# Kernel optimization log

Hardware: AMD Instinct MI355X
Metric: run time of the kernel (lower is better)

## Reference

```python
import jax, jax.numpy as jnp
import numpy as np


def setup_inputs() -> dict:
    key = jax.random.key(0)
    k1, k2, k3, k4, k5 = jax.random.split(key, 5)
    B, Tx, Ty, E, D = 8, 256, 256, 256, 256
    return {
        "encoder_out_seq": jax.random.normal(k1, (B, Tx, E), dtype=jnp.float32),
        "decoder_out_seq": jax.random.normal(k2, (B, Ty, D), dtype=jnp.float32),
        "W_a": jax.random.normal(k3, (E, E), dtype=jnp.float32) * 0.05,
        "U_a": jax.random.normal(k4, (D, E), dtype=jnp.float32) * 0.05,
        "V_a": jax.random.normal(k5, (E, 1), dtype=jnp.float32) * 0.05,
    }


def reference(encoder_out_seq, decoder_out_seq, W_a, U_a, V_a):
    # encoder_out_seq: [B, Tx, E], decoder_out_seq: [B, Ty, D]
    # Vectorized Bahdanau additive attention (the K.rnn scan is a fake
    # recurrence: each timestep only uses the per-step decoder input and the
    # constant encoder sequence).
    W_dot_s = jnp.einsum("bxe,ef->bxf", encoder_out_seq, W_a)   # [B, Tx, E]
    U_dot_h = jnp.einsum("byd,de->bye", decoder_out_seq, U_a)   # [B, Ty, E]
    # [B, Ty, Tx, E] broadcast add + tanh, then project with V_a -> [B, Ty, Tx]
    Ws_plus_Uh = jnp.tanh(W_dot_s[:, None, :, :] + U_dot_h[:, :, None, :])
    e = jnp.einsum("byxe,eo->byx", Ws_plus_Uh, V_a)             # [B, Ty, Tx]
    e = jax.nn.softmax(e, axis=-1)                               # softmax over Tx
    # context: weighted sum of encoder states -> [B, Ty, E]
    c = jnp.einsum("byx,bxe->bye", e, encoder_out_seq)
    return (c, e)
```

## Files before the change

### kernel.cpp

```cpp
#include <hip/hip_runtime.h>
#include <cstddef>
#include <stdint.h>

#define NB 8
#define TX 256
#define TY 256
#define NE 256

#define CSC 2.8853900817779268f

__device__ __forceinline__ void gload_lds16(const float* g, float* l) {
    __builtin_amdgcn_global_load_lds(
        (const __attribute__((address_space(1))) void*)g,
        (__attribute__((address_space(3))) void*)l,
        16, 0, 0);
}

__global__ __launch_bounds__(512) void prep_kernel(
    const float* __restrict__ enc, const float* __restrict__ dec,
    const float* __restrict__ Wa, const float* __restrict__ Ua,
    float* __restrict__ ZwT, float* __restrict__ Zu)
{
    const int tx = threadIdx.x;
    const int w  = threadIdx.y;
    const int tid = w * 64 + tx;
    int blk = blockIdx.x;
    const bool isU = blk >= 128;
    if (isU) blk -= 128;
    const int b  = blk >> 4;
    const int r0 = (blk & 15) * 16;

    __shared__ float rowsL[16 * NE];
    __shared__ float MbL[2][16 * NE];
    __shared__ float tL[16][260];

    const float* M = isU ? Ua : Wa;

    gload_lds16(M + tid * 4,        MbL[0] + w * 256);
    gload_lds16(M + 2048 + tid * 4, MbL[0] + 2048 + w * 256);
    const float* src = (isU ? dec : enc) + ((size_t)b * 256 + r0) * NE;
    ((float4*)rowsL)[tid]       = ((const float4*)src)[tid];
    ((float4*)rowsL)[tid + 512] = ((const float4*)src)[tid + 512];
    __syncthreads();

    const int e0 = tx * 4;
    const int rA = w * 2, rB = w * 2 + 1;
    float4 acc0 = make_float4(0.f, 0.f, 0.f, 0.f);
    float4 acc1 = make_float4(0.f, 0.f, 0.f, 0.f);
    const float* rowA = rowsL + rA * NE;
    const float* rowB = rowsL + rB * NE;

    for (int c = 0; c < 16; ++c) {
        if (c < 15) {
            const float* g = M + (size_t)(c + 1) * 4096;
            float* dst = MbL[(c + 1) & 1];
            gload_lds16(g + tid * 4,        dst + w * 256);
            gload_lds16(g + 2048 + tid * 4, dst + 2048 + w * 256);
        }
        const float* mb = MbL[c & 1] + e0;
        const int kbase = c * 16;
        #pragma unroll
        for (int j = 0; j < 16; ++j) {
            const float4 mw = *(const float4*)(mb + j * NE);
            const float a = rowA[kbase + j];
            const float d = rowB[kbase + j];
            acc0.x = __builtin_fmaf(a, mw.x, acc0.x);
            acc0.y = __builtin_fmaf(a, mw.y, acc0.y);
            acc0.z = __builtin_fmaf(a, mw.z, acc0.z);
            acc0.w = __builtin_fmaf(a, mw.w, acc0.w);
            acc1.x = __builtin_fmaf(d, mw.x, acc1.x);
            acc1.y = __builtin_fmaf(d, mw.y, acc1.y);
            acc1.z = __builtin_fmaf(d, mw.z, acc1.z);
            acc1.w = __builtin_fmaf(d, mw.w, acc1.w);
        }
        __syncthreads();
    }

    acc0.x = __builtin_amdgcn_exp2f(acc0.x * CSC);
    acc0.y = __builtin_amdgcn_exp2f(acc0.y * CSC);
    acc0.z = __builtin_amdgcn_exp2f(acc0.z * CSC);
    acc0.w = __builtin_amdgcn_exp2f(acc0.w * CSC);
    acc1.x = __builtin_amdgcn_exp2f(acc1.x * CSC);
    acc1.y = __builtin_amdgcn_exp2f(acc1.y * CSC);
    acc1.z = __builtin_amdgcn_exp2f(acc1.z * CSC);
    acc1.w = __builtin_amdgcn_exp2f(acc1.w * CSC);

    if (isU) {
        *(float4*)(Zu + ((size_t)b * TY + r0 + rA) * NE + e0) = acc0;
        *(float4*)(Zu + ((size_t)b * TY + r0 + rB) * NE + e0) = acc1;
    } else {
        *(float4*)&tL[rA][e0] = acc0;
        *(float4*)&tL[rB][e0] = acc1;
        __syncthreads();
        #pragma unroll
        for (int rep = 0; rep < 2; ++rep) {
            const int f4id = tid + rep * 512;
            const int e  = f4id >> 2;
            const int xq = (f4id & 3) * 4;
            float4 o;
            o.x = tL[xq + 0][e];
            o.y = tL[xq + 1][e];
            o.z = tL[xq + 2][e];
            o.w = tL[xq + 3][e];
            *(float4*)(ZwT + (size_t)b * NE * TX + (size_t)e * TX + r0 + xq) = o;
        }
    }
}

__global__ __launch_bounds__(512, 4) void attn_kernel(
    const float* __restrict__ enc, const float* __restrict__ ZwT,
    const float* __restrict__ Zu, const float* __restrict__ Va,
    float* __restrict__ c_out, float* __restrict__ e_out)
{
    const int tx = threadIdx.x;
    const int w  = threadIdx.y;
    const int tid = w * 64 + tx;
    const int b  = blockIdx.x & 7;
    const int y0 = (blockIdx.x >> 3) * 4;

    __shared__ float4 zu4L[NE];
    __shared__ float  vL[NE];
    __shared__ float4 accL[8][4][64];
    __shared__ float  pL4[TX][4];

    {
        const int e = tid & 255;
        if (tid < 256) {
            const float* zp = Zu + ((size_t)b * TY + y0) * NE + e;
            zu4L[e] = make_float4(zp[0], zp[NE], zp[2 * NE], zp[3 * NE]);
        } else {
            vL[e] = Va[e];
        }
    }
    __syncthreads();

    const float* wp = ZwT + (size_t)b * NE * TX + (size_t)(w * 32) * TX + tx * 4;
    const float4* zup = &zu4L[w * 32];
    const float*  vp  = &vL[w * 32];
    float4 acc0 = make_float4(0.f, 0.f, 0.f, 0.f);
    float4 acc1 = acc0, acc2 = acc0, acc3 = acc0;
    #pragma unroll 4
    for (int e = 0; e < 32; ++e) {
        const float4 zw  = *(const float4*)(wp + (size_t)e * TX);
        const float4 zu4 = zup[e];
        const float  v   = vp[e];
        acc0.x = __builtin_fmaf(v, __builtin_amdgcn_rcpf(__builtin_fmaf(zw.x, zu4.x, 1.f)), acc0.x);
        acc0.y = __builtin_fmaf(v, __builtin_amdgcn_rcpf(__builtin_fmaf(zw.y, zu4.x, 1.f)), acc0.y);
        acc0.z = __builtin_fmaf(v, __builtin_amdgcn_rcpf(__builtin_fmaf(zw.z, zu4.x, 1.f)), acc0.z);
        acc0.w = __builtin_fmaf(v, __builtin_amdgcn_rcpf(__builtin_fmaf(zw.w, zu4.x, 1.f)), acc0.w);
        acc1.x = __builtin_fmaf(v, __builtin_amdgcn_rcpf(__builtin_fmaf(zw.x, zu4.y, 1.f)), acc1.x);
        acc1.y = __builtin_fmaf(v, __builtin_amdgcn_rcpf(__builtin_fmaf(zw.y, zu4.y, 1.f)), acc1.y);
        acc1.z = __builtin_fmaf(v, __builtin_amdgcn_rcpf(__builtin_fmaf(zw.z, zu4.y, 1.f)), acc1.z);
        acc1.w = __builtin_fmaf(v, __builtin_amdgcn_rcpf(__builtin_fmaf(zw.w, zu4.y, 1.f)), acc1.w);
        acc2.x = __builtin_fmaf(v, __builtin_amdgcn_rcpf(__builtin_fmaf(zw.x, zu4.z, 1.f)), acc2.x);
        acc2.y = __builtin_fmaf(v, __builtin_amdgcn_rcpf(__builtin_fmaf(zw.y, zu4.z, 1.f)), acc2.y);
        acc2.z = __builtin_fmaf(v, __builtin_amdgcn_rcpf(__builtin_fmaf(zw.z, zu4.z, 1.f)), acc2.z);
        acc2.w = __builtin_fmaf(v, __builtin_amdgcn_rcpf(__builtin_fmaf(zw.w, zu4.z, 1.f)), acc2.w);
        acc3.x = __builtin_fmaf(v, __builtin_amdgcn_rcpf(__builtin_fmaf(zw.x, zu4.w, 1.f)), acc3.x);
        acc3.y = __builtin_fmaf(v, __builtin_amdgcn_rcpf(__builtin_fmaf(zw.y, zu4.w, 1.f)), acc3.y);
        acc3.z = __builtin_fmaf(v, __builtin_amdgcn_rcpf(__builtin_fmaf(zw.z, zu4.w, 1.f)), acc3.z);
        acc3.w = __builtin_fmaf(v, __builtin_amdgcn_rcpf(__builtin_fmaf(zw.w, zu4.w, 1.f)), acc3.w);
    }
    accL[w][0][tx] = acc0;
    accL[w][1][tx] = acc1;
    accL[w][2][tx] = acc2;
    accL[w][3][tx] = acc3;
    __syncthreads();

    const int yy = w & 3;
    float4 s = make_float4(0.f, 0.f, 0.f, 0.f);
    #pragma unroll
    for (int ww = 0; ww < 8; ++ww) {
        const float4 a = accL[ww][yy][tx];
        s.x += a.x; s.y += a.y; s.z += a.z; s.w += a.w;
    }
    s.x *= -2.f; s.y *= -2.f; s.z *= -2.f; s.w *= -2.f;

    float m = fmaxf(fmaxf(s.x, s.y), fmaxf(s.z, s.w));
    #pragma unroll
    for (int off = 32; off; off >>= 1) m = fmaxf(m, __shfl_xor(m, off));
    float4 p;
    p.x = __expf(s.x - m);
    p.y = __expf(s.y - m);
    p.z = __expf(s.z - m);
    p.w = __expf(s.w - m);
    float sum = (p.x + p.y) + (p.z + p.w);
    #pragma unroll
    for (int off = 32; off; off >>= 1) sum += __shfl_xor(sum, off);
    const float inv = __builtin_amdgcn_rcpf(sum);
    p.x *= inv; p.y *= inv; p.z *= inv; p.w *= inv;

    if (w < 4) {
        *(float4*)(e_out + ((size_t)b * TY + y0 + yy) * TX + tx * 4) = p;
        pL4[tx * 4 + 0][yy] = p.x;
        pL4[tx * 4 + 1][yy] = p.y;
        pL4[tx * 4 + 2][yy] = p.z;
        pL4[tx * 4 + 3][yy] = p.w;
    }
    __syncthreads();

    const float* ep = enc + (size_t)b * TX * NE + (size_t)(w * 32) * NE + tx * 4;
    float4 c0 = make_float4(0.f, 0.f, 0.f, 0.f);
    float4 c1 = c0, c2 = c0, c3 = c0;
    #pragma unroll 4
    for (int x = 0; x < 32; ++x) {
        const float4 ev = *(const float4*)(ep + (size_t)x * NE);
        const float4 p4 = *(const float4*)&pL4[w * 32 + x][0];
        c0.x = __builtin_fmaf(p4.x, ev.x, c0.x);
        c0.y = __builtin_fmaf(p4.x, ev.y, c0.y);
        c0.z = __builtin_fmaf(p4.x, ev.z, c0.z);
        c0.w = __builtin_fmaf(p4.x, ev.w, c0.w);
        c1.x = __builtin_fmaf(p4.y, ev.x, c1.x);
        c1.y = __builtin_fmaf(p4.y, ev.y, c1.y);
        c1.z = __builtin_fmaf(p4.y, ev.z, c1.z);
        c1.w = __builtin_fmaf(p4.y, ev.w, c1.w);
        c2.x = __builtin_fmaf(p4.z, ev.x, c2.x);
        c2.y = __builtin_fmaf(p4.z, ev.y, c2.y);
        c2.z = __builtin_fmaf(p4.z, ev.z, c2.z);
        c2.w = __builtin_fmaf(p4.z, ev.w, c2.w);
        c3.x = __builtin_fmaf(p4.w, ev.x, c3.x);
        c3.y = __builtin_fmaf(p4.w, ev.y, c3.y);
        c3.z = __builtin_fmaf(p4.w, ev.z, c3.z);
        c3.w = __builtin_fmaf(p4.w, ev.w, c3.w);
    }
    __syncthreads();
    accL[w][0][tx] = c0;
    accL[w][1][tx] = c1;
    accL[w][2][tx] = c2;
    accL[w][3][tx] = c3;
    __syncthreads();

    if (w < 4) {
        float4 cs = make_float4(0.f, 0.f, 0.f, 0.f);
        #pragma unroll
        for (int ww = 0; ww < 8; ++ww) {
            const float4 t = accL[ww][w][tx];
            cs.x += t.x; cs.y += t.y; cs.z += t.z; cs.w += t.w;
        }
        *(float4*)(c_out + ((size_t)b * TY + y0 + w) * NE + tx * 4) = cs;
    }
}

extern "C" void kernel_launch(void* const* d_in, const int* in_sizes, int n_in,
                              void* d_out, int out_size, void* d_ws, size_t ws_size,
                              hipStream_t stream) {
    const float* enc = (const float*)d_in[0];
    const float* dec = (const float*)d_in[1];
    const float* Wa  = (const float*)d_in[2];
    const float* Ua  = (const float*)d_in[3];
    const float* Va  = (const float*)d_in[4];

    float* c_out = (float*)d_out;
    float* e_out = (float*)d_out + (size_t)NB * TY * NE;

    float* ZwT = (float*)d_ws;
    float* Zu  = (float*)d_ws + (size_t)NB * NE * TX;

    prep_kernel<<<256, dim3(64, 8), 0, stream>>>(enc, dec, Wa, Ua, ZwT, Zu);
    attn_kernel<<<512, dim3(64, 8), 0, stream>>>(enc, ZwT, Zu, Va, c_out, e_out);
}
```

Before: 39.61 us.

## Process eight decoder rows per attention block and retile prep GEMM

The attention kernel now handles 8 decoder rows per block instead of 4, halving the grid to 256 blocks. Each ZwT and encoder load is reused across twice as many rows, and all 8 waves take part in the softmax, the stores and the context reduction. The prep kernel holds the input rows transposed in LDS, so each thread computes a 4-row by 2-column tile from float4 row reads. The trade-off is more registers per thread (occupancy hint lowered from 4 to 2), a larger LDS footprint and fewer blocks to spread across CUs.

```diff
diff --git a/kernel.cpp b/kernel.cpp
--- a/kernel.cpp
+++ b/kernel.cpp
@@ -30,25 +30,33 @@
     const int b  = blk >> 4;
     const int r0 = (blk & 15) * 16;
 
-    __shared__ float rowsL[16 * NE];
-    __shared__ float MbL[2][16 * NE];
+    const int rq = (w & 3) * 4;
+    const int eh = (w >> 2) * 128;
+    const int cc = eh + tx * 2;
+
+    __shared__ float rowsT[256][16];
+    __shared__ float MbL[2][16 * 256];
     __shared__ float tL[16][260];
 
     const float* M = isU ? Ua : Wa;
 
+    const float* src = (isU ? dec : enc) + ((size_t)b * 256 + r0) * NE;
+    #pragma unroll
+    for (int j = 0; j < 2; ++j) {
+        const int f   = tid + j * 512;
+        const int row = f & 15;
+        const int kq  = f >> 4;
+        const float4 v = ((const float4*)src)[row * 64 + kq];
+        rowsT[kq * 4 + 0][row] = v.x;
+        rowsT[kq * 4 + 1][row] = v.y;
+        rowsT[kq * 4 + 2][row] = v.z;
+        rowsT[kq * 4 + 3][row] = v.w;
+    }
     gload_lds16(M + tid * 4,        MbL[0] + w * 256);
     gload_lds16(M + 2048 + tid * 4, MbL[0] + 2048 + w * 256);
-    const float* src = (isU ? dec : enc) + ((size_t)b * 256 + r0) * NE;
-    ((float4*)rowsL)[tid]       = ((const float4*)src)[tid];
-    ((float4*)rowsL)[tid + 512] = ((const float4*)src)[tid + 512];
-    __syncthreads();
-
-    const int e0 = tx * 4;
-    const int rA = w * 2, rB = w * 2 + 1;
-    float4 acc0 = make_float4(0.f, 0.f, 0.f, 0.f);
-    float4 acc1 = make_float4(0.f, 0.f, 0.f, 0.f);
-    const float* rowA = rowsL + rA * NE;
-    const float* rowB = rowsL + rB * NE;
+    __syncthreads();
+
+    float2 a0 = make_float2(0.f, 0.f), a1 = a0, a2 = a0, a3 = a0;
 
     for (int c = 0; c < 16; ++c) {
         if (c < 15) {
@@ -57,57 +65,61 @@
             gload_lds16(g + tid * 4,        dst + w * 256);
             gload_lds16(g + 2048 + tid * 4, dst + 2048 + w * 256);
         }
-        const float* mb = MbL[c & 1] + e0;
+        const float* mb = MbL[c & 1] + cc;
         const int kbase = c * 16;
-        #pragma unroll
+        #pragma unroll 8
         for (int j = 0; j < 16; ++j) {
-            const float4 mw = *(const float4*)(mb + j * NE);
-            const float a = rowA[kbase + j];
-            const float d = rowB[kbase + j];
-            acc0.x = __builtin_fmaf(a, mw.x, acc0.x);
-            acc0.y = __builtin_fmaf(a, mw.y, acc0.y);
-            acc0.z = __builtin_fmaf(a, mw.z, acc0.z);
-            acc0.w = __builtin_fmaf(a, mw.w, acc0.w);
-            acc1.x = __builtin_fmaf(d, mw.x, acc1.x);
-            acc1.y = __builtin_fmaf(d, mw.y, acc1.y);
-            acc1.z = __builtin_fmaf(d, mw.z, acc1.z);
-            acc1.w = __builtin_fmaf(d, mw.w, acc1.w);
+            const float2 mw = *(const float2*)(mb + j * 256);
+            const float4 rv = *(const float4*)&rowsT[kbase + j][rq];
+            a0.x = __builtin_fmaf(rv.x, mw.x, a0.x);
+            a0.y = __builtin_fmaf(rv.x, mw.y, a0.y);
+            a1.x = __builtin_fmaf(rv.y, mw.x, a1.x);
+            a1.y = __builtin_fmaf(rv.y, mw.y, a1.y);
+            a2.x = __builtin_fmaf(rv.z, mw.x, a2.x);
+            a2.y = __builtin_fmaf(rv.z, mw.y, a2.y);
+            a3.x = __builtin_fmaf(rv.w, mw.x, a3.x);
+            a3.y = __builtin_fmaf(rv.w, mw.y, a3.y);
         }
         __syncthreads();
     }
 
-    acc0.x = __builtin_amdgcn_exp2f(acc0.x * CSC);
-    acc0.y = __builtin_amdgcn_exp2f(acc0.y * CSC);
-    acc0.z = __builtin_amdgcn_exp2f(acc0.z * CSC);
-    acc0.w = __builtin_amdgcn_exp2f(acc0.w * CSC);
-    acc1.x = __builtin_amdgcn_exp2f(acc1.x * CSC);
-    acc1.y = __builtin_amdgcn_exp2f(acc1.y * CSC);
-    acc1.z = __builtin_amdgcn_exp2f(acc1.z * CSC);
-    acc1.w = __builtin_amdgcn_exp2f(acc1.w * CSC);
+    a0.x = __builtin_amdgcn_exp2f(a0.x * CSC);
+    a0.y = __builtin_amdgcn_exp2f(a0.y * CSC);
+    a1.x = __builtin_amdgcn_exp2f(a1.x * CSC);
+    a1.y = __builtin_amdgcn_exp2f(a1.y * CSC);
+    a2.x = __builtin_amdgcn_exp2f(a2.x * CSC);
+    a2.y = __builtin_amdgcn_exp2f(a2.y * CSC);
+    a3.x = __builtin_amdgcn_exp2f(a3.x * CSC);
+    a3.y = __builtin_amdgcn_exp2f(a3.y * CSC);
 
     if (isU) {
-        *(float4*)(Zu + ((size_t)b * TY + r0 + rA) * NE + e0) = acc0;
-        *(float4*)(Zu + ((size_t)b * TY + r0 + rB) * NE + e0) = acc1;
+        const int rbase = r0 + rq;
+        *(float2*)(Zu + ((size_t)b * TY + rbase + 0) * NE + cc) = a0;
+        *(float2*)(Zu + ((size_t)b * TY + rbase + 1) * NE + cc) = a1;
+        *(float2*)(Zu + ((size_t)b * TY + rbase + 2) * NE + cc) = a2;
+        *(float2*)(Zu + ((size_t)b * TY + rbase + 3) * NE + cc) = a3;
     } else {
-        *(float4*)&tL[rA][e0] = acc0;
-        *(float4*)&tL[rB][e0] = acc1;
+        tL[rq + 0][cc] = a0.x; tL[rq + 0][cc + 1] = a0.y;
+        tL[rq + 1][cc] = a1.x; tL[rq + 1][cc + 1] = a1.y;
+        tL[rq + 2][cc] = a2.x; tL[rq + 2][cc + 1] = a2.y;
+        tL[rq + 3][cc] = a3.x; tL[rq + 3][cc + 1] = a3.y;
         __syncthreads();
         #pragma unroll
         for (int rep = 0; rep < 2; ++rep) {
-            const int f4id = tid + rep * 512;
-            const int e  = f4id >> 2;
-            const int xq = (f4id & 3) * 4;
+            const int f   = tid + rep * 512;
+            const int e   = f >> 2;
+            const int xq4 = (f & 3) * 4;
             float4 o;
-            o.x = tL[xq + 0][e];
-            o.y = tL[xq + 1][e];
-            o.z = tL[xq + 2][e];
-            o.w = tL[xq + 3][e];
-            *(float4*)(ZwT + (size_t)b * NE * TX + (size_t)e * TX + r0 + xq) = o;
-        }
-    }
-}
-
-__global__ __launch_bounds__(512, 4) void attn_kernel(
+            o.x = tL[xq4 + 0][e];
+            o.y = tL[xq4 + 1][e];
+            o.z = tL[xq4 + 2][e];
+            o.w = tL[xq4 + 3][e];
+            *(float4*)(ZwT + ((size_t)b * NE + e) * TX + r0 + xq4) = o;
+        }
+    }
+}
+
+__global__ __launch_bounds__(512, 2) void attn_kernel(
     const float* __restrict__ enc, const float* __restrict__ ZwT,
     const float* __restrict__ Zu, const float* __restrict__ Va,
     float* __restrict__ c_out, float* __restrict__ e_out)
@@ -116,62 +128,57 @@
     const int w  = threadIdx.y;
     const int tid = w * 64 + tx;
     const int b  = blockIdx.x & 7;
-    const int y0 = (blockIdx.x >> 3) * 4;
-
-    __shared__ float4 zu4L[NE];
+    const int y0 = (blockIdx.x >> 3) * 8;
+    const int y  = y0 + w;
+
+    __shared__ float4 zuLo[NE];
+    __shared__ float4 zuHi[NE];
     __shared__ float  vL[NE];
-    __shared__ float4 accL[8][4][64];
-    __shared__ float  pL4[TX][4];
+    __shared__ float4 accL[8][8][64];
+    __shared__ float  pLT[8][TX];
 
     {
         const int e = tid & 255;
+        const float* zp = Zu + ((size_t)b * TY + y0) * NE + e;
         if (tid < 256) {
-            const float* zp = Zu + ((size_t)b * TY + y0) * NE + e;
-            zu4L[e] = make_float4(zp[0], zp[NE], zp[2 * NE], zp[3 * NE]);
+            zuLo[e] = make_float4(zp[0], zp[NE], zp[2 * NE], zp[3 * NE]);
+            vL[e] = Va[e];
         } else {
-            vL[e] = Va[e];
+            zuHi[e] = make_float4(zp[4 * NE], zp[5 * NE], zp[6 * NE], zp[7 * NE]);
         }
     }
     __syncthreads();
 
     const float* wp = ZwT + (size_t)b * NE * TX + (size_t)(w * 32) * TX + tx * 4;
-    const float4* zup = &zu4L[w * 32];
-    const float*  vp  = &vL[w * 32];
-    float4 acc0 = make_float4(0.f, 0.f, 0.f, 0.f);
-    float4 acc1 = acc0, acc2 = acc0, acc3 = acc0;
+    float4 a0 = make_float4(0.f, 0.f, 0.f, 0.f);
+    float4 a1 = a0, a2 = a0, a3 = a0, a4 = a0, a5 = a0, a6 = a0, a7 = a0;
+
+#define SC(A, ZU) \
+    A.x = __builtin_fmaf(v, __builtin_amdgcn_rcpf(__builtin_fmaf(zw.x, ZU, 1.f)), A.x); \
+    A.y = __builtin_fmaf(v, __builtin_amdgcn_rcpf(__builtin_fmaf(zw.y, ZU, 1.f)), A.y); \
+    A.z = __builtin_fmaf(v, __builtin_amdgcn_rcpf(__builtin_fmaf(zw.z, ZU, 1.f)), A.z); \
+    A.w = __builtin_fmaf(v, __builtin_amdgcn_rcpf(__builtin_fmaf(zw.w, ZU, 1.f)), A.w);
+
     #pragma unroll 4
     for (int e = 0; e < 32; ++e) {
-        const float4 zw  = *(const float4*)(wp + (size_t)e * TX);
-        const float4 zu4 = zup[e];
-        const float  v   = vp[e];
-        acc0.x = __builtin_fmaf(v, __builtin_amdgcn_rcpf(__builtin_fmaf(zw.x, zu4.x, 1.f)), acc0.x);
-        acc0.y = __builtin_fmaf(v, __builtin_amdgcn_rcpf(__builtin_fmaf(zw.y, zu4.x, 1.f)), acc0.y);
-        acc0.z = __builtin_fmaf(v, __builtin_amdgcn_rcpf(__builtin_fmaf(zw.z, zu4.x, 1.f)), acc0.z);
-        acc0.w = __builtin_fmaf(v, __builtin_amdgcn_rcpf(__builtin_fmaf(zw.w, zu4.x, 1.f)), acc0.w);
-        acc1.x = __builtin_fmaf(v, __builtin_amdgcn_rcpf(__builtin_fmaf(zw.x, zu4.y, 1.f)), acc1.x);
-        acc1.y = __builtin_fmaf(v, __builtin_amdgcn_rcpf(__builtin_fmaf(zw.y, zu4.y, 1.f)), acc1.y);
-        acc1.z = __builtin_fmaf(v, __builtin_amdgcn_rcpf(__builtin_fmaf(zw.z, zu4.y, 1.f)), acc1.z);
-        acc1.w = __builtin_fmaf(v, __builtin_amdgcn_rcpf(__builtin_fmaf(zw.w, zu4.y, 1.f)), acc1.w);
-        acc2.x = __builtin_fmaf(v, __builtin_amdgcn_rcpf(__builtin_fmaf(zw.x, zu4.z, 1.f)), acc2.x);
-        acc2.y = __builtin_fmaf(v, __builtin_amdgcn_rcpf(__builtin_fmaf(zw.y, zu4.z, 1.f)), acc2.y);
-        acc2.z = __builtin_fmaf(v, __builtin_amdgcn_rcpf(__builtin_fmaf(zw.z, zu4.z, 1.f)), acc2.z);
-        acc2.w = __builtin_fmaf(v, __builtin_amdgcn_rcpf(__builtin_fmaf(zw.w, zu4.z, 1.f)), acc2.w);
-        acc3.x = __builtin_fmaf(v, __builtin_amdgcn_rcpf(__builtin_fmaf(zw.x, zu4.w, 1.f)), acc3.x);
-        acc3.y = __builtin_fmaf(v, __builtin_amdgcn_rcpf(__builtin_fmaf(zw.y, zu4.w, 1.f)), acc3.y);
-        acc3.z = __builtin_fmaf(v, __builtin_amdgcn_rcpf(__builtin_fmaf(zw.z, zu4.w, 1.f)), acc3.z);
-        acc3.w = __builtin_fmaf(v, __builtin_amdgcn_rcpf(__builtin_fmaf(zw.w, zu4.w, 1.f)), acc3.w);
-    }
-    accL[w][0][tx] = acc0;
-    accL[w][1][tx] = acc1;
-    accL[w][2][tx] = acc2;
-    accL[w][3][tx] = acc3;
-    __syncthreads();
-
-    const int yy = w & 3;
+        const float4 zw = *(const float4*)(wp + (size_t)e * TX);
+        const float4 zl = zuLo[w * 32 + e];
+        const float4 zh = zuHi[w * 32 + e];
+        const float  v  = vL[w * 32 + e];
+        SC(a0, zl.x) SC(a1, zl.y) SC(a2, zl.z) SC(a3, zl.w)
+        SC(a4, zh.x) SC(a5, zh.y) SC(a6, zh.z) SC(a7, zh.w)
+    }
+#undef SC
+    accL[w][0][tx] = a0; accL[w][1][tx] = a1;
+    accL[w][2][tx] = a2; accL[w][3][tx] = a3;
+    accL[w][4][tx] = a4; accL[w][5][tx] = a5;
+    accL[w][6][tx] = a6; accL[w][7][tx] = a7;
+    __syncthreads();
+
     float4 s = make_float4(0.f, 0.f, 0.f, 0.f);
     #pragma unroll
     for (int ww = 0; ww < 8; ++ww) {
-        const float4 a = accL[ww][yy][tx];
+        const float4 a = accL[ww][w][tx];
         s.x += a.x; s.y += a.y; s.z += a.z; s.w += a.w;
     }
     s.x *= -2.f; s.y *= -2.f; s.z *= -2.f; s.w *= -2.f;
@@ -190,55 +197,60 @@
     const float inv = __builtin_amdgcn_rcpf(sum);
     p.x *= inv; p.y *= inv; p.z *= inv; p.w *= inv;
 
-    if (w < 4) {
-        *(float4*)(e_out + ((size_t)b * TY + y0 + yy) * TX + tx * 4) = p;
-        pL4[tx * 4 + 0][yy] = p.x;
-        pL4[tx * 4 + 1][yy] = p.y;
-        pL4[tx * 4 + 2][yy] = p.z;
-        pL4[tx * 4 + 3][yy] = p.w;
-    }
+    *(float4*)(e_out + ((size_t)b * TY + y) * TX + tx * 4) = p;
+    *(float4*)&pLT[w][tx * 4] = p;
     __syncthreads();
 
     const float* ep = enc + (size_t)b * TX * NE + (size_t)(w * 32) * NE + tx * 4;
     float4 c0 = make_float4(0.f, 0.f, 0.f, 0.f);
-    float4 c1 = c0, c2 = c0, c3 = c0;
-    #pragma unroll 4
-    for (int x = 0; x < 32; ++x) {
-        const float4 ev = *(const float4*)(ep + (size_t)x * NE);
-        const float4 p4 = *(const float4*)&pL4[w * 32 + x][0];
-        c0.x = __builtin_fmaf(p4.x, ev.x, c0.x);
-        c0.y = __builtin_fmaf(p4.x, ev.y, c0.y);
-        c0.z = __builtin_fmaf(p4.x, ev.z, c0.z);
-        c0.w = __builtin_fmaf(p4.x, ev.w, c0.w);
-        c1.x = __builtin_fmaf(p4.y, ev.x, c1.x);
-        c1.y = __builtin_fmaf(p4.y, ev.y, c1.y);
-        c1.z = __builtin_fmaf(p4.y, ev.z, c1.z);
-        c1.w = __builtin_fmaf(p4.y, ev.w, c1.w);
-        c2.x = __builtin_fmaf(p4.z, ev.x, c2.x);
-        c2.y = __builtin_fmaf(p4.z, ev.y, c2.y);
-        c2.z = __builtin_fmaf(p4.z, ev.z, c2.z);
-        c2.w = __builtin_fmaf(p4.z, ev.w, c2.w);
-        c3.x = __builtin_fmaf(p4.w, ev.x, c3.x);
-        c3.y = __builtin_fmaf(p4.w, ev.y, c3.y);
-        c3.z = __builtin_fmaf(p4.w, ev.z, c3.z);
-        c3.w = __builtin_fmaf(p4.w, ev.w, c3.w);
-    }
-    __syncthreads();
-    accL[w][0][tx] = c0;
-    accL[w][1][tx] = c1;
-    accL[w][2][tx] = c2;
-    accL[w][3][tx] = c3;
-    __syncthreads();
-
-    if (w < 4) {
-        float4 cs = make_float4(0.f, 0.f, 0.f, 0.f);
-        #pragma unroll
-        for (int ww = 0; ww < 8; ++ww) {
-            const float4 t = accL[ww][w][tx];
-            cs.x += t.x; cs.y += t.y; cs.z += t.z; cs.w += t.w;
-        }
-        *(float4*)(c_out + ((size_t)b * TY + y0 + w) * NE + tx * 4) = cs;
-    }
+    float4 c1 = c0, c2 = c0, c3 = c0, c4 = c0, c5 = c0, c6 = c0, c7 = c0;
+
+#define CTXY(CY, RP, EV) \
+    CY.x = __builtin_fmaf(RP, EV.x, CY.x); \
+    CY.y = __builtin_fmaf(RP, EV.y, CY.y); \
+    CY.z = __builtin_fmaf(RP, EV.z, CY.z); \
+    CY.w = __builtin_fmaf(RP, EV.w, CY.w);
+#define CTXI(COMP, EV) \
+    CTXY(c0, rp0.COMP, EV) CTXY(c1, rp1.COMP, EV) CTXY(c2, rp2.COMP, EV) CTXY(c3, rp3.COMP, EV) \
+    CTXY(c4, rp4.COMP, EV) CTXY(c5, rp5.COMP, EV) CTXY(c6, rp6.COMP, EV) CTXY(c7, rp7.COMP, EV)
+
+    #pragma unroll 2
+    for (int g = 0; g < 8; ++g) {
+        const int xg = g * 4;
+        const float4 rp0 = *(const float4*)&pLT[0][w * 32 + xg];
+        const float4 rp1 = *(const float4*)&pLT[1][w * 32 + xg];
+        const float4 rp2 = *(const float4*)&pLT[2][w * 32 + xg];
+        const float4 rp3 = *(const float4*)&pLT[3][w * 32 + xg];
+        const float4 rp4 = *(const float4*)&pLT[4][w * 32 + xg];
+        const float4 rp5 = *(const float4*)&pLT[5][w * 32 + xg];
+        const float4 rp6 = *(const float4*)&pLT[6][w * 32 + xg];
+        const float4 rp7 = *(const float4*)&pLT[7][w * 32 + xg];
+        const float4 ev0 = *(const float4*)(ep + (size_t)(xg + 0) * NE);
+        const float4 ev1 = *(const float4*)(ep + (size_t)(xg + 1) * NE);
+        const float4 ev2 = *(const float4*)(ep + (size_t)(xg + 2) * NE);
+        const float4 ev3 = *(const float4*)(ep + (size_t)(xg + 3) * NE);
+        CTXI(x, ev0)
+        CTXI(y, ev1)
+        CTXI(z, ev2)
+        CTXI(w, ev3)
+    }
+#undef CTXI
+#undef CTXY
+
+    __syncthreads();
+    accL[w][0][tx] = c0; accL[w][1][tx] = c1;
+    accL[w][2][tx] = c2; accL[w][3][tx] = c3;
+    accL[w][4][tx] = c4; accL[w][5][tx] = c5;
+    accL[w][6][tx] = c6; accL[w][7][tx] = c7;
+    __syncthreads();
+
+    float4 cs = make_float4(0.f, 0.f, 0.f, 0.f);
+    #pragma unroll
+    for (int ww = 0; ww < 8; ++ww) {
+        const float4 t = accL[ww][w][tx];
+        cs.x += t.x; cs.y += t.y; cs.z += t.z; cs.w += t.w;
+    }
+    *(float4*)(c_out + ((size_t)b * TY + y) * NE + tx * 4) = cs;
 }
 
 extern "C" void kernel_launch(void* const* d_in, const int* in_sizes, int n_in,
@@ -257,5 +269,5 @@
     float* Zu  = (float*)d_ws + (size_t)NB * NE * TX;
 
     prep_kernel<<<256, dim3(64, 8), 0, stream>>>(enc, dec, Wa, Ua, ZwT, Zu);
-    attn_kernel<<<512, dim3(64, 8), 0, stream>>>(enc, ZwT, Zu, Va, c_out, e_out);
-}
+    attn_kernel<<<256, dim3(64, 8), 0, stream>>>(enc, ZwT, Zu, Va, c_out, e_out);
+}
```

Result: slower. 41.44 us (+4.6%).
